# Optimization experiments

Hardware: AMD Instinct MI355X
Metric: run time of the kernel (lower is better)

Reference implementation:

```python
import jax, jax.numpy as jnp
import numpy as np

NUM_EMBEDDINGS = 8192
EMBEDDING_DIM = 64
N_VOXELS = 32768


def setup_inputs() -> dict:
    key = jax.random.key(0)
    k1, k2 = jax.random.split(key)
    z = jax.random.normal(k1, (N_VOXELS, EMBEDDING_DIM), dtype=jnp.float32)
    codebook = jax.random.normal(k2, (NUM_EMBEDDINGS, EMBEDDING_DIM), dtype=jnp.float32)
    return {"z": z, "codebook": codebook}


def reference(z, codebook):
    # Squared euclidean distances [N, K]; argmin is identical to argmin of cdist.
    # d2 = ||z||^2 - 2 z E^T + ||E||^2
    z_sq = jnp.sum(z * z, axis=1, keepdims=True)            # [N, 1]
    e_sq = jnp.sum(codebook * codebook, axis=1)              # [K]
    d2 = z_sq - 2.0 * (z @ codebook.T) + e_sq[None, :]       # [N, K]
    encoding_indices = jnp.argmin(d2, axis=1)                # [N] int

    quantized_feats = codebook[encoding_indices]             # [N, D] gather

    sg = jax.lax.stop_gradient
    commitment_loss = jnp.mean((z - sg(quantized_feats)) ** 2)
    vq_loss = jnp.mean((quantized_feats - sg(z)) ** 2)

    # Straight-through estimator
    quantized = z + sg(quantized_feats - z)                  # [N, D]

    return quantized, vq_loss, commitment_loss, encoding_indices
```

## Files before the change

### kernel.cpp

```cpp
#include <hip/hip_runtime.h>
#include <math.h>

#define N_VOX 32768
#define N_EMB 8192
#define DIM 64
#define NCHUNK 8
#define CODES_PER_CHUNK (N_EMB / NCHUNK)
#define TILES_PER_CHUNK (CODES_PER_CHUNK / 32)
#define NTILES (N_EMB / 32)
#define TILE_BYTES 8192
#define CHUNK_BYTES (TILES_PER_CHUNK * TILE_BYTES)

typedef _Float16 half8 __attribute__((ext_vector_type(8)));
typedef float floatx16 __attribute__((ext_vector_type(16)));

#define FP16_MIN_NORMAL 6.1035156e-5f
#define LO_SCALE 2048.0f

__global__ __launch_bounds__(256) void cbprep_kernel(const float* __restrict__ cb,
                                                     char* __restrict__ stream,
                                                     float* __restrict__ c0arr) {
    __shared__ float red[256];
    int tid  = threadIdx.x;
    int l    = tid & 63;
    int o    = tid >> 6;
    int m    = l & 31;
    int kg   = l >> 5;
    int tile = blockIdx.x;
    char* tbase = stream + (size_t)tile * TILE_BYTES;
    int code = tile * 32 + m;

    const float* p = cb + (size_t)code * DIM + o * 16 + kg * 8;
    float ss = 0.f;
    half8 h, lo;
    #pragma unroll
    for (int j = 0; j < 8; ++j) {
        float x = p[j];
        ss = fmaf(x, x, ss);
        _Float16 hi = (_Float16)x;
        float hf = (float)hi;
        if (fabsf(hf) < FP16_MIN_NORMAL) { hi = (_Float16)0.f; hf = 0.f; }
        h[j]  = hi;
        lo[j] = (_Float16)((x - hf) * LO_SCALE);
    }
    *(half8*)(tbase +        o * 1024 + l * 16) = h;
    *(half8*)(tbase + 4096 + o * 1024 + l * 16) = lo;

    red[tid] = ss;
    __syncthreads();
    if (tid < 32) {
        float s = 0.f;
        #pragma unroll
        for (int q = 0; q < 8; ++q) s += red[tid + q * 32];
        c0arr[tile * 32 + tid] = -1024.0f * s;
    }
}

__global__ __launch_bounds__(512) void scan_kernel(const float* __restrict__ z,
                                                   const char* __restrict__ stream,
                                                   const float* __restrict__ c0arr,
                                                   float* __restrict__ cand_val,
                                                   int* __restrict__ cand_idx) {
    __shared__ __align__(16) char lds[4 * TILE_BYTES + CODES_PER_CHUNK * 4];
    float* c0_lds = (float*)(lds + 4 * TILE_BYTES);
    int tid   = threadIdx.x;
    int l     = tid & 63;
    int w     = tid >> 6;
    int chunk = blockIdx.x & (NCHUNK - 1);
    int rg    = blockIdx.x >> 3;
    int m     = l & 31;
    int kg    = l >> 5;
    int rowBase = rg * 256 + w * 32;

    half8 zh[4], zl[4], zhs[4];
    const float* zrow = z + (size_t)(rowBase + m) * DIM + kg * 8;
    #pragma unroll
    for (int o = 0; o < 4; ++o) {
        const float* p = zrow + o * 16;
        #pragma unroll
        for (int j = 0; j < 8; ++j) {
            float x = p[j];
            _Float16 hi = (_Float16)x;
            float hf = (float)hi;
            if (fabsf(hf) < FP16_MIN_NORMAL) { hi = (_Float16)0.f; hf = 0.f; }
            zh[o][j] = hi;
            zl[o][j] = (_Float16)((x - hf) * LO_SCALE);
        }
        zhs[o] = zh[o] * (_Float16)2048.0f;
    }

    const char*  sbase = stream + (size_t)chunk * CHUNK_BYTES;
    const float* c0p   = c0arr + chunk * CODES_PER_CHUNK;

    float best[16];
    int   bt[16];
    #pragma unroll
    for (int i = 0; i < 16; ++i) { best[i] = -3.4e38f; bt[i] = 0; }

#define STAGE(gt, lb)                                                              \
    do {                                                                           \
        const char* _g = (gt) + w * 1024 + l * 16;                                 \
        char*       _d = (lb) + w * 1024 + l * 16;                                 \
        __builtin_amdgcn_global_load_lds(                                          \
            (const __attribute__((address_space(1))) void*)_g,                     \
            (__attribute__((address_space(3))) void*)_d, 16, 0, 0);                \
    } while (0)

    STAGE(sbase,                        lds);
    STAGE(sbase + (size_t)TILE_BYTES,   lds + TILE_BYTES);
    STAGE(sbase + 2 * (size_t)TILE_BYTES, lds + 2 * TILE_BYTES);
    c0_lds[tid]       = c0p[tid];
    c0_lds[tid + 512] = c0p[tid + 512];
    __syncthreads();

    for (int t = 0; t < TILES_PER_CHUNK; ++t) {
        if (t < TILES_PER_CHUNK - 2)
            asm volatile("s_waitcnt vmcnt(2)" ::: "memory");
        else if (t == TILES_PER_CHUNK - 2)
            asm volatile("s_waitcnt vmcnt(1)" ::: "memory");
        else
            asm volatile("s_waitcnt vmcnt(0)" ::: "memory");
        __builtin_amdgcn_s_barrier();
        asm volatile("" ::: "memory");

        if (t + 3 < TILES_PER_CHUNK)
            STAGE(sbase + (size_t)(t + 3) * TILE_BYTES,
                  lds + ((t + 3) & 3) * TILE_BYTES);

        const char* lb = lds + (t & 3) * TILE_BYTES;
        float c0 = c0_lds[t * 32 + m];
        half8 bh[4], bl[4];
        #pragma unroll
        for (int o = 0; o < 4; ++o) {
            bh[o] = *(const half8*)(lb +        o * 1024 + l * 16);
            bl[o] = *(const half8*)(lb + 4096 + o * 1024 + l * 16);
        }

        floatx16 acc;
        #pragma unroll
        for (int i = 0; i < 16; ++i) acc[i] = c0;
        #pragma unroll
        for (int o = 0; o < 4; ++o) {
            acc = __builtin_amdgcn_mfma_f32_32x32x16_f16(zhs[o], bh[o], acc, 0, 0, 0);
            acc = __builtin_amdgcn_mfma_f32_32x32x16_f16(zl[o],  bh[o], acc, 0, 0, 0);
            acc = __builtin_amdgcn_mfma_f32_32x32x16_f16(zh[o],  bl[o], acc, 0, 0, 0);
        }
        #pragma unroll
        for (int i = 0; i < 16; ++i)
            if (acc[i] > best[i]) { best[i] = acc[i]; bt[i] = t; }
    }
#undef STAGE

    #pragma unroll
    for (int i = 0; i < 16; ++i) {
        float v  = best[i];
        int   id = bt[i] * 32 + m;
        #pragma unroll
        for (int off = 1; off < 32; off <<= 1) {
            float ov = __shfl_xor(v, off, 64);
            int   oi = __shfl_xor(id, off, 64);
            if (ov > v || (ov == v && oi < id)) { v = ov; id = oi; }
        }
        if (m == 0) {
            int row = rowBase + (i & 3) + 8 * (i >> 2) + 4 * kg;
            cand_val[chunk * N_VOX + row] = v;
            cand_idx[chunk * N_VOX + row] = chunk * CODES_PER_CHUNK + id;
        }
    }
}

__global__ __launch_bounds__(256) void finalize_kernel(const float* __restrict__ z,
                                                       const float* __restrict__ cb,
                                                       const float* __restrict__ cand_val,
                                                       const int* __restrict__ cand_idx,
                                                       float* __restrict__ out,
                                                       float* __restrict__ partials) {
    int g    = blockIdx.x * 256 + threadIdx.x;
    int row  = g >> 3;
    int c    = g & 7;

    float v  = cand_val[c * N_VOX + row];
    int   id = cand_idx[c * N_VOX + row];
    #pragma unroll
    for (int off = 1; off < 8; off <<= 1) {
        float ov = __shfl_xor(v, off, 8);
        int   oi = __shfl_xor(id, off, 8);
        if (ov > v || (ov == v && oi < id)) { v = ov; id = oi; }
    }

    if (c == 0)
        out[(size_t)N_VOX * DIM + 2 + row] = (float)id;

    const float4* zp = (const float4*)(z  + (size_t)row * DIM + c * 8);
    const float4* qp = (const float4*)(cb + (size_t)id  * DIM + c * 8);
    float4*       op = (float4*)(out + (size_t)row * DIM + c * 8);
    float ss = 0.f;
    #pragma unroll
    for (int d = 0; d < 2; ++d) {
        float4 zt = zp[d], qt = qp[d];
        float dx = qt.x - zt.x, dy = qt.y - zt.y;
        float dz = qt.z - zt.z, dw = qt.w - zt.w;
        float4 o;
        o.x = zt.x + dx; o.y = zt.y + dy;
        o.z = zt.z + dz; o.w = zt.w + dw;
        op[d] = o;
        ss += dx*dx + dy*dy + dz*dz + dw*dw;
    }

    __shared__ float red[256];
    red[threadIdx.x] = ss;
    __syncthreads();
    #pragma unroll
    for (int s = 128; s > 0; s >>= 1) {
        if (threadIdx.x < s) red[threadIdx.x] += red[threadIdx.x + s];
        __syncthreads();
    }
    if (threadIdx.x == 0) partials[blockIdx.x] = red[0];
}

__global__ __launch_bounds__(256) void loss_kernel(const float* __restrict__ partials,
                                                   float* __restrict__ out) {
    __shared__ float red[256];
    red[threadIdx.x] = (partials[threadIdx.x]       + partials[threadIdx.x + 256])
                     + (partials[threadIdx.x + 512] + partials[threadIdx.x + 768]);
    __syncthreads();
    #pragma unroll
    for (int st = 128; st > 0; st >>= 1) {
        if (threadIdx.x < st) red[threadIdx.x] += red[threadIdx.x + st];
        __syncthreads();
    }
    if (threadIdx.x == 0) {
        float mean = red[0] / (float)((size_t)N_VOX * DIM);
        out[(size_t)N_VOX * DIM + 0] = mean;
        out[(size_t)N_VOX * DIM + 1] = mean;
    }
}

extern "C" void kernel_launch(void* const* d_in, const int* in_sizes, int n_in,
                              void* d_out, int out_size, void* d_ws, size_t ws_size,
                              hipStream_t stream) {
    const float* z  = (const float*)d_in[0];
    const float* cb = (const float*)d_in[1];
    float* out = (float*)d_out;

    char*  bstream  = (char*)d_ws;
    float* c0arr    = (float*)(bstream + (size_t)NTILES * TILE_BYTES);
    float* cand_val = c0arr + N_EMB;
    int*   cand_idx = (int*)(cand_val + (size_t)NCHUNK * N_VOX);
    float* partials = (float*)(cand_idx + (size_t)NCHUNK * N_VOX);

    cbprep_kernel  <<<dim3(NTILES), dim3(256), 0, stream>>>(cb, bstream, c0arr);
    scan_kernel    <<<dim3((N_VOX / 256) * NCHUNK), dim3(512), 0, stream>>>(z, bstream, c0arr, cand_val, cand_idx);
    finalize_kernel<<<dim3(N_VOX * 8 / 256), dim3(256), 0, stream>>>(z, cb, cand_val, cand_idx, out, partials);
    loss_kernel    <<<1, 256, 0, stream>>>(partials, out);
}
```

Before: 175.7 us.

## Process two 32-row groups per wave to reuse codebook tile fragments

The scan kernel now runs 256 threads per block, and each wave handles 64 voxel rows as two 32-row MFMA tiles instead of one. Each codebook tile's fp16 hi/lo fragments are read from LDS once and fed to both row groups, which halves LDS reads and barriers per unit of MFMA work. Each wave issues twice the global-to-LDS staging loads, and the vmcnt waits are adjusted to match. The MFMA chains are wrapped in s_setprio. The trade-off is about double the per-thread register use for z fragments and running minima, which could lower occupancy or cause spills.

```diff
diff --git a/kernel.cpp b/kernel.cpp
--- a/kernel.cpp
+++ b/kernel.cpp
@@ -56,11 +56,11 @@
     }
 }
 
-__global__ __launch_bounds__(512) void scan_kernel(const float* __restrict__ z,
-                                                   const char* __restrict__ stream,
-                                                   const float* __restrict__ c0arr,
-                                                   float* __restrict__ cand_val,
-                                                   int* __restrict__ cand_idx) {
+__global__ __launch_bounds__(256, 2) void scan_kernel(const float* __restrict__ z,
+                                                      const char* __restrict__ stream,
+                                                      const float* __restrict__ c0arr,
+                                                      float* __restrict__ cand_val,
+                                                      int* __restrict__ cand_idx) {
     __shared__ __align__(16) char lds[4 * TILE_BYTES + CODES_PER_CHUNK * 4];
     float* c0_lds = (float*)(lds + 4 * TILE_BYTES);
     int tid   = threadIdx.x;
@@ -70,54 +70,73 @@
     int rg    = blockIdx.x >> 3;
     int m     = l & 31;
     int kg    = l >> 5;
-    int rowBase = rg * 256 + w * 32;
-
-    half8 zh[4], zl[4], zhs[4];
-    const float* zrow = z + (size_t)(rowBase + m) * DIM + kg * 8;
-    #pragma unroll
-    for (int o = 0; o < 4; ++o) {
-        const float* p = zrow + o * 16;
-        #pragma unroll
-        for (int j = 0; j < 8; ++j) {
-            float x = p[j];
-            _Float16 hi = (_Float16)x;
-            float hf = (float)hi;
-            if (fabsf(hf) < FP16_MIN_NORMAL) { hi = (_Float16)0.f; hf = 0.f; }
-            zh[o][j] = hi;
-            zl[o][j] = (_Float16)((x - hf) * LO_SCALE);
-        }
-        zhs[o] = zh[o] * (_Float16)2048.0f;
+    int rowBase = rg * 256 + w * 64;
+
+    half8 zh0[4], zl0[4], zhs0[4], zh1[4], zl1[4], zhs1[4];
+    {
+        const float* zr0 = z + (size_t)(rowBase + m)      * DIM + kg * 8;
+        const float* zr1 = z + (size_t)(rowBase + 32 + m) * DIM + kg * 8;
+        #pragma unroll
+        for (int o = 0; o < 4; ++o) {
+            const float* p0 = zr0 + o * 16;
+            const float* p1 = zr1 + o * 16;
+            #pragma unroll
+            for (int j = 0; j < 8; ++j) {
+                float x = p0[j];
+                _Float16 hi = (_Float16)x;
+                float hf = (float)hi;
+                if (fabsf(hf) < FP16_MIN_NORMAL) { hi = (_Float16)0.f; hf = 0.f; }
+                zh0[o][j] = hi;
+                zl0[o][j] = (_Float16)((x - hf) * LO_SCALE);
+                float y = p1[j];
+                _Float16 hj = (_Float16)y;
+                float hg = (float)hj;
+                if (fabsf(hg) < FP16_MIN_NORMAL) { hj = (_Float16)0.f; hg = 0.f; }
+                zh1[o][j] = hj;
+                zl1[o][j] = (_Float16)((y - hg) * LO_SCALE);
+            }
+            zhs0[o] = zh0[o] * (_Float16)2048.0f;
+            zhs1[o] = zh1[o] * (_Float16)2048.0f;
+        }
     }
 
     const char*  sbase = stream + (size_t)chunk * CHUNK_BYTES;
     const float* c0p   = c0arr + chunk * CODES_PER_CHUNK;
 
-    float best[16];
-    int   bt[16];
-    #pragma unroll
-    for (int i = 0; i < 16; ++i) { best[i] = -3.4e38f; bt[i] = 0; }
+    float best0[16], best1[16];
+    int   bt0[16],   bt1[16];
+    #pragma unroll
+    for (int i = 0; i < 16; ++i) {
+        best0[i] = -3.4e38f; bt0[i] = 0;
+        best1[i] = -3.4e38f; bt1[i] = 0;
+    }
 
 #define STAGE(gt, lb)                                                              \
     do {                                                                           \
-        const char* _g = (gt) + w * 1024 + l * 16;                                 \
-        char*       _d = (lb) + w * 1024 + l * 16;                                 \
+        const char* _g = (gt) + w * 2048 + l * 16;                                 \
+        char*       _d = (lb) + w * 2048 + l * 16;                                 \
         __builtin_amdgcn_global_load_lds(                                          \
             (const __attribute__((address_space(1))) void*)_g,                     \
             (__attribute__((address_space(3))) void*)_d, 16, 0, 0);                \
+        __builtin_amdgcn_global_load_lds(                                          \
+            (const __attribute__((address_space(1))) void*)(_g + 1024),            \
+            (__attribute__((address_space(3))) void*)(_d + 1024), 16, 0, 0);       \
     } while (0)
 
-    STAGE(sbase,                        lds);
-    STAGE(sbase + (size_t)TILE_BYTES,   lds + TILE_BYTES);
+    STAGE(sbase,                          lds);
+    STAGE(sbase + (size_t)TILE_BYTES,     lds + TILE_BYTES);
     STAGE(sbase + 2 * (size_t)TILE_BYTES, lds + 2 * TILE_BYTES);
     c0_lds[tid]       = c0p[tid];
+    c0_lds[tid + 256] = c0p[tid + 256];
     c0_lds[tid + 512] = c0p[tid + 512];
+    c0_lds[tid + 768] = c0p[tid + 768];
     __syncthreads();
 
     for (int t = 0; t < TILES_PER_CHUNK; ++t) {
         if (t < TILES_PER_CHUNK - 2)
+            asm volatile("s_waitcnt vmcnt(4)" ::: "memory");
+        else if (t == TILES_PER_CHUNK - 2)
             asm volatile("s_waitcnt vmcnt(2)" ::: "memory");
-        else if (t == TILES_PER_CHUNK - 2)
-            asm volatile("s_waitcnt vmcnt(1)" ::: "memory");
         else
             asm volatile("s_waitcnt vmcnt(0)" ::: "memory");
         __builtin_amdgcn_s_barrier();
@@ -136,25 +155,42 @@
             bl[o] = *(const half8*)(lb + 4096 + o * 1024 + l * 16);
         }
 
-        floatx16 acc;
-        #pragma unroll
-        for (int i = 0; i < 16; ++i) acc[i] = c0;
+        floatx16 acc0;
+        #pragma unroll
+        for (int i = 0; i < 16; ++i) acc0[i] = c0;
+        __builtin_amdgcn_s_setprio(1);
         #pragma unroll
         for (int o = 0; o < 4; ++o) {
-            acc = __builtin_amdgcn_mfma_f32_32x32x16_f16(zhs[o], bh[o], acc, 0, 0, 0);
-            acc = __builtin_amdgcn_mfma_f32_32x32x16_f16(zl[o],  bh[o], acc, 0, 0, 0);
-            acc = __builtin_amdgcn_mfma_f32_32x32x16_f16(zh[o],  bl[o], acc, 0, 0, 0);
-        }
+            acc0 = __builtin_amdgcn_mfma_f32_32x32x16_f16(zhs0[o], bh[o], acc0, 0, 0, 0);
+            acc0 = __builtin_amdgcn_mfma_f32_32x32x16_f16(zl0[o],  bh[o], acc0, 0, 0, 0);
+            acc0 = __builtin_amdgcn_mfma_f32_32x32x16_f16(zh0[o],  bl[o], acc0, 0, 0, 0);
+        }
+        __builtin_amdgcn_s_setprio(0);
         #pragma unroll
         for (int i = 0; i < 16; ++i)
-            if (acc[i] > best[i]) { best[i] = acc[i]; bt[i] = t; }
+            if (acc0[i] > best0[i]) { best0[i] = acc0[i]; bt0[i] = t; }
+
+        floatx16 acc1;
+        #pragma unroll
+        for (int i = 0; i < 16; ++i) acc1[i] = c0;
+        __builtin_amdgcn_s_setprio(1);
+        #pragma unroll
+        for (int o = 0; o < 4; ++o) {
+            acc1 = __builtin_amdgcn_mfma_f32_32x32x16_f16(zhs1[o], bh[o], acc1, 0, 0, 0);
+            acc1 = __builtin_amdgcn_mfma_f32_32x32x16_f16(zl1[o],  bh[o], acc1, 0, 0, 0);
+            acc1 = __builtin_amdgcn_mfma_f32_32x32x16_f16(zh1[o],  bl[o], acc1, 0, 0, 0);
+        }
+        __builtin_amdgcn_s_setprio(0);
+        #pragma unroll
+        for (int i = 0; i < 16; ++i)
+            if (acc1[i] > best1[i]) { best1[i] = acc1[i]; bt1[i] = t; }
     }
 #undef STAGE
 
     #pragma unroll
     for (int i = 0; i < 16; ++i) {
-        float v  = best[i];
-        int   id = bt[i] * 32 + m;
+        float v  = best0[i];
+        int   id = bt0[i] * 32 + m;
         #pragma unroll
         for (int off = 1; off < 32; off <<= 1) {
             float ov = __shfl_xor(v, off, 64);
@@ -163,6 +199,22 @@
         }
         if (m == 0) {
             int row = rowBase + (i & 3) + 8 * (i >> 2) + 4 * kg;
+            cand_val[chunk * N_VOX + row] = v;
+            cand_idx[chunk * N_VOX + row] = chunk * CODES_PER_CHUNK + id;
+        }
+    }
+    #pragma unroll
+    for (int i = 0; i < 16; ++i) {
+        float v  = best1[i];
+        int   id = bt1[i] * 32 + m;
+        #pragma unroll
+        for (int off = 1; off < 32; off <<= 1) {
+            float ov = __shfl_xor(v, off, 64);
+            int   oi = __shfl_xor(id, off, 64);
+            if (ov > v || (ov == v && oi < id)) { v = ov; id = oi; }
+        }
+        if (m == 0) {
+            int row = rowBase + 32 + (i & 3) + 8 * (i >> 2) + 4 * kg;
             cand_val[chunk * N_VOX + row] = v;
             cand_idx[chunk * N_VOX + row] = chunk * CODES_PER_CHUNK + id;
         }
@@ -250,7 +302,7 @@
     float* partials = (float*)(cand_idx + (size_t)NCHUNK * N_VOX);
 
     cbprep_kernel  <<<dim3(NTILES), dim3(256), 0, stream>>>(cb, bstream, c0arr);
-    scan_kernel    <<<dim3((N_VOX / 256) * NCHUNK), dim3(512), 0, stream>>>(z, bstream, c0arr, cand_val, cand_idx);
+    scan_kernel    <<<dim3((N_VOX / 256) * NCHUNK), dim3(256), 0, stream>>>(z, bstream, c0arr, cand_val, cand_idx);
     finalize_kernel<<<dim3(N_VOX * 8 / 256), dim3(256), 0, stream>>>(z, cb, cand_val, cand_idx, out, partials);
     loss_kernel    <<<1, 256, 0, stream>>>(partials, out);
 }
```

After: 190.7 us. 1.09x slower.

## Stage codebook tiles in groups of four with double buffering and MFMA priority

Applied to the files above, without the earlier changes.

The per-tile wait and barrier in the scan loop is replaced by a two-group LDS ring of 8 tiles. The next group of four tiles is prefetched while the current four are computed, with only one __syncthreads per group. s_setprio is raised around the MFMA chain so math issue takes precedence over other waves. In exchange, LDS per block roughly doubles, which can reduce how many blocks fit on a CU. The design also relies on __syncthreads draining the outstanding LDS-direct loads.

```diff
diff --git a/kernel.cpp b/kernel.cpp
--- a/kernel.cpp
+++ b/kernel.cpp
@@ -61,8 +61,8 @@
                                                    const float* __restrict__ c0arr,
                                                    float* __restrict__ cand_val,
                                                    int* __restrict__ cand_idx) {
-    __shared__ __align__(16) char lds[4 * TILE_BYTES + CODES_PER_CHUNK * 4];
-    float* c0_lds = (float*)(lds + 4 * TILE_BYTES);
+    __shared__ __align__(16) char lds[8 * TILE_BYTES + CODES_PER_CHUNK * 4];
+    float* c0_lds = (float*)(lds + 8 * TILE_BYTES);
     int tid   = threadIdx.x;
     int l     = tid & 63;
     int w     = tid >> 6;
@@ -106,48 +106,53 @@
             (__attribute__((address_space(3))) void*)_d, 16, 0, 0);                \
     } while (0)
 
-    STAGE(sbase,                        lds);
-    STAGE(sbase + (size_t)TILE_BYTES,   lds + TILE_BYTES);
-    STAGE(sbase + 2 * (size_t)TILE_BYTES, lds + 2 * TILE_BYTES);
+    #pragma unroll
+    for (int u = 0; u < 4; ++u)
+        STAGE(sbase + (size_t)u * TILE_BYTES, lds + u * TILE_BYTES);
     c0_lds[tid]       = c0p[tid];
     c0_lds[tid + 512] = c0p[tid + 512];
     __syncthreads();
 
-    for (int t = 0; t < TILES_PER_CHUNK; ++t) {
-        if (t < TILES_PER_CHUNK - 2)
-            asm volatile("s_waitcnt vmcnt(2)" ::: "memory");
-        else if (t == TILES_PER_CHUNK - 2)
-            asm volatile("s_waitcnt vmcnt(1)" ::: "memory");
-        else
-            asm volatile("s_waitcnt vmcnt(0)" ::: "memory");
-        __builtin_amdgcn_s_barrier();
-        asm volatile("" ::: "memory");
-
-        if (t + 3 < TILES_PER_CHUNK)
-            STAGE(sbase + (size_t)(t + 3) * TILE_BYTES,
-                  lds + ((t + 3) & 3) * TILE_BYTES);
-
-        const char* lb = lds + (t & 3) * TILE_BYTES;
-        float c0 = c0_lds[t * 32 + m];
-        half8 bh[4], bl[4];
-        #pragma unroll
-        for (int o = 0; o < 4; ++o) {
-            bh[o] = *(const half8*)(lb +        o * 1024 + l * 16);
-            bl[o] = *(const half8*)(lb + 4096 + o * 1024 + l * 16);
-        }
-
-        floatx16 acc;
-        #pragma unroll
-        for (int i = 0; i < 16; ++i) acc[i] = c0;
-        #pragma unroll
-        for (int o = 0; o < 4; ++o) {
-            acc = __builtin_amdgcn_mfma_f32_32x32x16_f16(zhs[o], bh[o], acc, 0, 0, 0);
-            acc = __builtin_amdgcn_mfma_f32_32x32x16_f16(zl[o],  bh[o], acc, 0, 0, 0);
-            acc = __builtin_amdgcn_mfma_f32_32x32x16_f16(zh[o],  bl[o], acc, 0, 0, 0);
-        }
-        #pragma unroll
-        for (int i = 0; i < 16; ++i)
-            if (acc[i] > best[i]) { best[i] = acc[i]; bt[i] = t; }
+    for (int s = 0; s < TILES_PER_CHUNK / 4; ++s) {
+        int base = s * 4;
+        if (s < TILES_PER_CHUNK / 4 - 1) {
+            #pragma unroll
+            for (int u = 0; u < 4; ++u) {
+                int tt = base + 4 + u;
+                STAGE(sbase + (size_t)tt * TILE_BYTES,
+                      lds + (size_t)(tt & 7) * TILE_BYTES);
+            }
+        }
+
+        #pragma unroll 1
+        for (int u = 0; u < 4; ++u) {
+            int t = base + u;
+            const char* lb = lds + (size_t)(t & 7) * TILE_BYTES;
+            float c0 = c0_lds[t * 32 + m];
+            half8 bh[4], bl[4];
+            #pragma unroll
+            for (int o = 0; o < 4; ++o) {
+                bh[o] = *(const half8*)(lb +        o * 1024 + l * 16);
+                bl[o] = *(const half8*)(lb + 4096 + o * 1024 + l * 16);
+            }
+
+            floatx16 acc;
+            #pragma unroll
+            for (int i = 0; i < 16; ++i) acc[i] = c0;
+            __builtin_amdgcn_s_setprio(1);
+            #pragma unroll
+            for (int o = 0; o < 4; ++o) {
+                acc = __builtin_amdgcn_mfma_f32_32x32x16_f16(zhs[o], bh[o], acc, 0, 0, 0);
+                acc = __builtin_amdgcn_mfma_f32_32x32x16_f16(zl[o],  bh[o], acc, 0, 0, 0);
+                acc = __builtin_amdgcn_mfma_f32_32x32x16_f16(zh[o],  bl[o], acc, 0, 0, 0);
+            }
+            __builtin_amdgcn_s_setprio(0);
+            #pragma unroll
+            for (int i = 0; i < 16; ++i)
+                if (acc[i] > best[i]) { best[i] = acc[i]; bt[i] = t; }
+        }
+
+        __syncthreads();
     }
 #undef STAGE
 
```

Result: slower. 193.3 us (+10.0%).

## Switch scan kernel from 32x32x16 to 16x16x32 MFMA tiles

Applied to the files above, without the earlier changes.

Replaces the 32x32x16 fp16 MFMA with four 16x16x32 MFMA accumulators per 32x32 tile. This re-maps z fragments and LDS codebook reads to the new operand layout and shortens the final argmin shuffle reduction to 16 lanes. The aim is higher MFMA throughput, since 16x16x32 issues more FLOPs per cycle on CDNA3/4, and more independent accumulator chains. In exchange it adds more MFMA instructions with data dependencies to schedule, a different LDS read pattern that may hit bank conflicts, and depends on the fragment layout being correct.

```diff
diff --git a/kernel.cpp b/kernel.cpp
--- a/kernel.cpp
+++ b/kernel.cpp
@@ -12,7 +12,7 @@
 #define CHUNK_BYTES (TILES_PER_CHUNK * TILE_BYTES)
 
 typedef _Float16 half8 __attribute__((ext_vector_type(8)));
-typedef float floatx16 __attribute__((ext_vector_type(16)));
+typedef float floatx4 __attribute__((ext_vector_type(4)));
 
 #define FP16_MIN_NORMAL 6.1035156e-5f
 #define LO_SCALE 2048.0f
@@ -25,10 +25,10 @@
     int l    = tid & 63;
     int o    = tid >> 6;
     int m    = l & 31;
-    int kg   = l >> 5;
     int tile = blockIdx.x;
     char* tbase = stream + (size_t)tile * TILE_BYTES;
     int code = tile * 32 + m;
+    int kg   = l >> 5;
 
     const float* p = cb + (size_t)code * DIM + o * 16 + kg * 8;
     float ss = 0.f;
@@ -68,25 +68,27 @@
     int w     = tid >> 6;
     int chunk = blockIdx.x & (NCHUNK - 1);
     int rg    = blockIdx.x >> 3;
-    int m     = l & 31;
-    int kg    = l >> 5;
+    int lr    = l & 15;
+    int lq    = l >> 4;
     int rowBase = rg * 256 + w * 32;
 
-    half8 zh[4], zl[4], zhs[4];
-    const float* zrow = z + (size_t)(rowBase + m) * DIM + kg * 8;
-    #pragma unroll
-    for (int o = 0; o < 4; ++o) {
-        const float* p = zrow + o * 16;
-        #pragma unroll
-        for (int j = 0; j < 8; ++j) {
-            float x = p[j];
-            _Float16 hi = (_Float16)x;
-            float hf = (float)hi;
-            if (fabsf(hf) < FP16_MIN_NORMAL) { hi = (_Float16)0.f; hf = 0.f; }
-            zh[o][j] = hi;
-            zl[o][j] = (_Float16)((x - hf) * LO_SCALE);
+    half8 zh[2][2], zl[2][2], zhs[2][2];
+    #pragma unroll
+    for (int r = 0; r < 2; ++r) {
+        #pragma unroll
+        for (int h = 0; h < 2; ++h) {
+            const float* p = z + (size_t)(rowBase + r * 16 + lr) * DIM + h * 32 + lq * 8;
+            #pragma unroll
+            for (int j = 0; j < 8; ++j) {
+                float x = p[j];
+                _Float16 hi = (_Float16)x;
+                float hf = (float)hi;
+                if (fabsf(hf) < FP16_MIN_NORMAL) { hi = (_Float16)0.f; hf = 0.f; }
+                zh[r][h][j] = hi;
+                zl[r][h][j] = (_Float16)((x - hf) * LO_SCALE);
+            }
+            zhs[r][h] = zh[r][h] * (_Float16)2048.0f;
         }
-        zhs[o] = zh[o] * (_Float16)2048.0f;
     }
 
     const char*  sbase = stream + (size_t)chunk * CHUNK_BYTES;
@@ -106,8 +108,8 @@
             (__attribute__((address_space(3))) void*)_d, 16, 0, 0);                \
     } while (0)
 
-    STAGE(sbase,                        lds);
-    STAGE(sbase + (size_t)TILE_BYTES,   lds + TILE_BYTES);
+    STAGE(sbase,                          lds);
+    STAGE(sbase + (size_t)TILE_BYTES,     lds + TILE_BYTES);
     STAGE(sbase + 2 * (size_t)TILE_BYTES, lds + 2 * TILE_BYTES);
     c0_lds[tid]       = c0p[tid];
     c0_lds[tid + 512] = c0p[tid + 512];
@@ -128,43 +130,77 @@
                   lds + ((t + 3) & 3) * TILE_BYTES);
 
         const char* lb = lds + (t & 3) * TILE_BYTES;
-        float c0 = c0_lds[t * 32 + m];
-        half8 bh[4], bl[4];
-        #pragma unroll
-        for (int o = 0; o < 4; ++o) {
-            bh[o] = *(const half8*)(lb +        o * 1024 + l * 16);
-            bl[o] = *(const half8*)(lb + 4096 + o * 1024 + l * 16);
+        const char* bp = lb + 512 * lq + 16 * lr;
+        half8 bh00 = *(const half8*)(bp +    0);
+        half8 bh10 = *(const half8*)(bp +  256);
+        half8 bh01 = *(const half8*)(bp + 2048);
+        half8 bh11 = *(const half8*)(bp + 2304);
+        half8 bl00 = *(const half8*)(bp + 4096);
+        half8 bl10 = *(const half8*)(bp + 4352);
+        half8 bl01 = *(const half8*)(bp + 6144);
+        half8 bl11 = *(const half8*)(bp + 6400);
+        float c00 = c0_lds[t * 32 + lr];
+        float c01 = c0_lds[t * 32 + 16 + lr];
+
+        floatx4 a00 = {c00, c00, c00, c00};
+        floatx4 a01 = {c01, c01, c01, c01};
+        floatx4 a10 = {c00, c00, c00, c00};
+        floatx4 a11 = {c01, c01, c01, c01};
+
+        a00 = __builtin_amdgcn_mfma_f32_16x16x32_f16(zhs[0][0], bh00, a00, 0, 0, 0);
+        a01 = __builtin_amdgcn_mfma_f32_16x16x32_f16(zhs[0][0], bh10, a01, 0, 0, 0);
+        a10 = __builtin_amdgcn_mfma_f32_16x16x32_f16(zhs[1][0], bh00, a10, 0, 0, 0);
+        a11 = __builtin_amdgcn_mfma_f32_16x16x32_f16(zhs[1][0], bh10, a11, 0, 0, 0);
+        a00 = __builtin_amdgcn_mfma_f32_16x16x32_f16(zl[0][0],  bh00, a00, 0, 0, 0);
+        a01 = __builtin_amdgcn_mfma_f32_16x16x32_f16(zl[0][0],  bh10, a01, 0, 0, 0);
+        a10 = __builtin_amdgcn_mfma_f32_16x16x32_f16(zl[1][0],  bh00, a10, 0, 0, 0);
+        a11 = __builtin_amdgcn_mfma_f32_16x16x32_f16(zl[1][0],  bh10, a11, 0, 0, 0);
+        a00 = __builtin_amdgcn_mfma_f32_16x16x32_f16(zh[0][0],  bl00, a00, 0, 0, 0);
+        a01 = __builtin_amdgcn_mfma_f32_16x16x32_f16(zh[0][0],  bl10, a01, 0, 0, 0);
+        a10 = __builtin_amdgcn_mfma_f32_16x16x32_f16(zh[1][0],  bl00, a10, 0, 0, 0);
+        a11 = __builtin_amdgcn_mfma_f32_16x16x32_f16(zh[1][0],  bl10, a11, 0, 0, 0);
+        a00 = __builtin_amdgcn_mfma_f32_16x16x32_f16(zhs[0][1], bh01, a00, 0, 0, 0);
+        a01 = __builtin_amdgcn_mfma_f32_16x16x32_f16(zhs[0][1], bh11, a01, 0, 0, 0);
+        a10 = __builtin_amdgcn_mfma_f32_16x16x32_f16(zhs[1][1], bh01, a10, 0, 0, 0);
+        a11 = __builtin_amdgcn_mfma_f32_16x16x32_f16(zhs[1][1], bh11, a11, 0, 0, 0);
+        a00 = __builtin_amdgcn_mfma_f32_16x16x32_f16(zl[0][1],  bh01, a00, 0, 0, 0);
+        a01 = __builtin_amdgcn_mfma_f32_16x16x32_f16(zl[0][1],  bh11, a01, 0, 0, 0);
+        a10 = __builtin_amdgcn_mfma_f32_16x16x32_f16(zl[1][1],  bh01, a10, 0, 0, 0);
+        a11 = __builtin_amdgcn_mfma_f32_16x16x32_f16(zl[1][1],  bh11, a11, 0, 0, 0);
+        a00 = __builtin_amdgcn_mfma_f32_16x16x32_f16(zh[0][1],  bl01, a00, 0, 0, 0);
+        a01 = __builtin_amdgcn_mfma_f32_16x16x32_f16(zh[0][1],  bl11, a01, 0, 0, 0);
+        a10 = __builtin_amdgcn_mfma_f32_16x16x32_f16(zh[1][1],  bl01, a10, 0, 0, 0);
+        a11 = __builtin_amdgcn_mfma_f32_16x16x32_f16(zh[1][1],  bl11, a11, 0, 0, 0);
+
+        #pragma unroll
+        for (int i = 0; i < 4; ++i) {
+            if (a00[i] > best[ 0 + i]) { best[ 0 + i] = a00[i]; bt[ 0 + i] = t; }
+            if (a01[i] > best[ 4 + i]) { best[ 4 + i] = a01[i]; bt[ 4 + i] = t; }
+            if (a10[i] > best[ 8 + i]) { best[ 8 + i] = a10[i]; bt[ 8 + i] = t; }
+            if (a11[i] > best[12 + i]) { best[12 + i] = a11[i]; bt[12 + i] = t; }
         }
-
-        floatx16 acc;
-        #pragma unroll
-        for (int i = 0; i < 16; ++i) acc[i] = c0;
-        #pragma unroll
-        for (int o = 0; o < 4; ++o) {
-            acc = __builtin_amdgcn_mfma_f32_32x32x16_f16(zhs[o], bh[o], acc, 0, 0, 0);
-            acc = __builtin_amdgcn_mfma_f32_32x32x16_f16(zl[o],  bh[o], acc, 0, 0, 0);
-            acc = __builtin_amdgcn_mfma_f32_32x32x16_f16(zh[o],  bl[o], acc, 0, 0, 0);
-        }
-        #pragma unroll
-        for (int i = 0; i < 16; ++i)
-            if (acc[i] > best[i]) { best[i] = acc[i]; bt[i] = t; }
     }
 #undef STAGE
 
     #pragma unroll
-    for (int i = 0; i < 16; ++i) {
-        float v  = best[i];
-        int   id = bt[i] * 32 + m;
-        #pragma unroll
-        for (int off = 1; off < 32; off <<= 1) {
-            float ov = __shfl_xor(v, off, 64);
-            int   oi = __shfl_xor(id, off, 64);
-            if (ov > v || (ov == v && oi < id)) { v = ov; id = oi; }
-        }
-        if (m == 0) {
-            int row = rowBase + (i & 3) + 8 * (i >> 2) + 4 * kg;
-            cand_val[chunk * N_VOX + row] = v;
-            cand_idx[chunk * N_VOX + row] = chunk * CODES_PER_CHUNK + id;
+    for (int r = 0; r < 2; ++r) {
+        #pragma unroll
+        for (int i = 0; i < 4; ++i) {
+            float v0 = best[r * 8 + i];     int id0 = bt[r * 8 + i] * 32 + lr;
+            float v1 = best[r * 8 + 4 + i]; int id1 = bt[r * 8 + 4 + i] * 32 + 16 + lr;
+            float v = v0; int id = id0;
+            if (v1 > v || (v1 == v && id1 < id)) { v = v1; id = id1; }
+            #pragma unroll
+            for (int off = 1; off < 16; off <<= 1) {
+                float ov = __shfl_xor(v, off, 64);
+                int   oi = __shfl_xor(id, off, 64);
+                if (ov > v || (ov == v && oi < id)) { v = ov; id = oi; }
+            }
+            if (lr == 0) {
+                int row = rowBase + r * 16 + 4 * lq + i;
+                cand_val[chunk * N_VOX + row] = v;
+                cand_idx[chunk * N_VOX + row] = chunk * CODES_PER_CHUNK + id;
+            }
         }
     }
 }
```

Result: faster. 157.7 us (median of 2 runs) (-10.2%).
